# Performance work log

Hardware: AMD Instinct MI355X
Metric: run time of the kernel (lower is better)

The kernel has to match this reference:

```python
import jax, jax.numpy as jnp
import numpy as np

HIDDEN = 128
M_DIM = 128
N_NODES = 50000
N_EDGES = 600000

def _linear_params(key, fan_in, fan_out):
    k1, k2 = jax.random.split(key)
    bound = 1.0 / np.sqrt(fan_in)
    W = jax.random.uniform(k1, (fan_in, fan_out), jnp.float32, -bound, bound)
    b = jax.random.uniform(k2, (fan_out,), jnp.float32, -bound, bound)
    return W, b

def setup_inputs() -> dict:
    key = jax.random.key(0)
    ks = jax.random.split(key, 10)
    h = jax.random.normal(ks[0], (N_NODES, HIDDEN), jnp.float32)
    x = jax.random.normal(ks[1], (N_NODES, 3), jnp.float32)
    edge_index = jax.random.randint(ks[2], (2, N_EDGES), 0, N_NODES, jnp.int64)
    We1, be1 = _linear_params(ks[3], 2 * HIDDEN + 1, M_DIM)
    We2, be2 = _linear_params(ks[4], M_DIM, M_DIM)
    Wg, bg = _linear_params(ks[5], M_DIM, 1)
    Wn1, bn1 = _linear_params(ks[6], HIDDEN + M_DIM, HIDDEN)
    Wn2, bn2 = _linear_params(ks[7], HIDDEN, HIDDEN)
    Wc1, bc1 = _linear_params(ks[8], M_DIM, M_DIM)
    Wc2, bc2 = _linear_params(ks[9], M_DIM, 1)
    return {"h": h, "x": x, "edge_index": edge_index,
            "We1": We1, "be1": be1, "We2": We2, "be2": be2,
            "Wg": Wg, "bg": bg,
            "Wn1": Wn1, "bn1": bn1, "Wn2": Wn2, "bn2": bn2,
            "Wc1": Wc1, "bc1": bc1, "Wc2": Wc2, "bc2": bc2}

def reference(h, x, edge_index, We1, be1, We2, be2, Wg, bg,
              Wn1, bn1, Wn2, bn2, Wc1, bc1, Wc2, bc2):
    silu = jax.nn.silu
    row, col = edge_index[0], edge_index[1]
    N = h.shape[0]
    # gather endpoints
    x_j = x[row]          # [E, 3]
    x_i = x[col]          # [E, 3]
    coord_diff = x_i - x_j
    dist = jnp.linalg.norm(coord_diff, axis=-1, keepdims=True)  # [E, 1]
    h_j = h[row]          # [E, H]
    h_i = h[col]          # [E, H]
    msg_inputs = jnp.concatenate([h_i, h_j, dist], axis=-1)     # [E, 2H+1]
    # edge MLP: Linear -> SiLU -> Linear -> SiLU
    m_ij = silu(silu(msg_inputs @ We1 + be1) @ We2 + be2)       # [E, M]
    gate = jax.nn.sigmoid(m_ij @ Wg + bg)                       # [E, 1]
    m_ij = m_ij * gate
    # scatter-add aggregation over destination nodes
    m_aggr = jax.ops.segment_sum(m_ij, col, num_segments=N)     # [N, M]
    node_input = jnp.concatenate([h, m_aggr], axis=-1)          # [N, H+M]
    delta_h = silu(node_input @ Wn1 + bn1) @ Wn2 + bn2
    h_out = h + delta_h
    # coordinate update
    coor_weights = (silu(m_ij @ Wc1 + bc1) @ Wc2 + bc2)         # [E, 1]
    coord_updates = coord_diff * coor_weights                   # [E, 3]
    coord_aggr = jax.ops.segment_sum(coord_updates, col, num_segments=N)
    x_out = x + coord_aggr
    return (h_out, x_out)
```

## Files before the change

kernel.cpp:

```cpp
#include <hip/hip_runtime.h>
#include <cmath>

#define HID 128

typedef __attribute__((ext_vector_type(8))) short bf16x8;
typedef __attribute__((ext_vector_type(4))) float f32x4;

__device__ __forceinline__ unsigned short f2bf(float f) {
    union { float f; unsigned int i; } c; c.f = f;
    unsigned int r = c.i + 0x7fffu + ((c.i >> 16) & 1u);
    return (unsigned short)(r >> 16);
}
__device__ __forceinline__ unsigned cvt_pk(float lo, float hi) {
    unsigned r;
    asm("v_cvt_pk_bf16_f32 %0, %1, %2" : "=v"(r) : "v"(lo), "v"(hi));
    return r;
}
__device__ __forceinline__ float silu_f(float v) {
    float t = __builtin_amdgcn_exp2f(-1.44269504f * v);
    return v * __builtin_amdgcn_rcpf(1.0f + t);
}
__device__ __forceinline__ float sigmoid_f(float v) {
    return __builtin_amdgcn_rcpf(1.0f + __builtin_amdgcn_exp2f(-1.44269504f * v));
}
typedef __fp16 fp16x2 __attribute__((ext_vector_type(2)));
__device__ __forceinline__ void atomic_pk_add_f16(void* p, float lo, float hi) {
    union { fp16x2 h; unsigned u; } cv;
    cv.h = __builtin_amdgcn_cvt_pkrtz(lo, hi);
    unsigned long long a = (unsigned long long)p;
    asm volatile("global_atomic_pk_add_f16 %0, %1, off" :: "v"(a), "v"(cv.u) : "memory");
}

__global__ __launch_bounds__(256) void egnn_prep(
    const float* __restrict__ We1, const float* __restrict__ We2,
    const float* __restrict__ Wc1, const float* __restrict__ Wn1,
    const float* __restrict__ Wn2,
    short* __restrict__ We1p, short* __restrict__ We2p, short* __restrict__ Wc1p,
    short* __restrict__ Wn1p, short* __restrict__ Wn2p)
{
    int t = blockIdx.x * 256 + threadIdx.x;
    int frag = t >> 6, lane = t & 63;
    if (frag >= 224) return;
    const float* W; short* dst; int KC, f;
    if (frag < 64)       { W = We1; dst = We1p; KC = 8; f = frag; }
    else if (frag < 96)  { W = We2; dst = We2p; KC = 4; f = frag - 64; }
    else if (frag < 128) { W = Wc1; dst = Wc1p; KC = 4; f = frag - 96; }
    else if (frag < 192) { W = Wn1; dst = Wn1p; KC = 8; f = frag - 128; }
    else                 { W = Wn2; dst = Wn2p; KC = 4; f = frag - 192; }
    int nt = f / KC, kc = f % KC;
    int n = nt * 16 + (lane & 15);
    short* d = dst + (((size_t)nt * KC + kc) * 64 + lane) * 8;
    #pragma unroll
    for (int j = 0; j < 8; ++j) {
        int k = kc * 32 + ((lane >> 4) << 2) + (j & 3) + ((j >> 2) << 4);
        d[j] = (short)f2bf(W[(size_t)k * HID + n]);
    }
}

__global__ __launch_bounds__(256) void egnn_edge_mfma(
    const float* __restrict__ h, const float* __restrict__ x,
    const int* __restrict__ ei, int E,
    const short* __restrict__ We1p, const float* __restrict__ We1,
    const float* __restrict__ be1,
    const short* __restrict__ We2p, const float* __restrict__ be2,
    const float* __restrict__ Wg, const float* __restrict__ bg,
    const short* __restrict__ Wc1p, const float* __restrict__ bc1,
    const float* __restrict__ Wc2, const float* __restrict__ bc2,
    short* __restrict__ m16, float* __restrict__ coord_aggr)
{
    __shared__ short sStage[64 * 256];
    __shared__ float s_be1[128], s_w256[128], s_be2[128];
    __shared__ float s_wg[128], s_bc1[128], s_wc2[128];
    __shared__ int   s_col[64], s_row[64];

    const int tid  = threadIdx.x;
    const int lane = tid & 63;
    const int w    = tid >> 6;
    const int l15  = lane & 15;
    const int g    = lane >> 4;
    const int e0   = blockIdx.x * 64;

    if (tid < 64) {
        s_row[tid] = ei[e0 + tid];
        s_col[tid] = ei[E + e0 + tid];
    }
    if (tid < 128) {
        s_be1[tid]  = be1[tid];
        s_w256[tid] = We1[(size_t)256 * HID + tid];
        s_be2[tid]  = be2[tid];
        s_wg[tid]   = Wg[tid];
        s_bc1[tid]  = bc1[tid];
        s_wc2[tid]  = Wc2[tid];
    }
    __syncthreads();

    #pragma unroll
    for (int it = 0; it < 16; ++it) {
        int e = w + 4 * it;
        int q = lane;
        int node = (q < 32) ? s_col[e] : s_row[e];
        float4 v = *(const float4*)&h[(size_t)node * HID + (size_t)(q & 31) * 4];
        uint2 pk;
        pk.x = cvt_pk(v.x, v.y);
        pk.y = cvt_pk(v.z, v.w);
        *(uint2*)((char*)sStage + e * 512 + ((q * 8) ^ ((e & 7) << 4))) = pk;
    }

    const int eloc = w * 16 + l15;
    const int nr = s_row[eloc], nc = s_col[eloc];
    float dx = x[nc * 3 + 0] - x[nr * 3 + 0];
    float dy = x[nc * 3 + 1] - x[nr * 3 + 1];
    float dz = x[nc * 3 + 2] - x[nr * 3 + 2];
    float dist = sqrtf(dx * dx + dy * dy + dz * dz);
    __syncthreads();

    const char* stageRow = (const char*)sStage + eloc * 512;
    const int sw = (eloc & 7) << 4;
    const bf16x8* A1 = (const bf16x8*)We1p;
    const bf16x8* A2 = (const bf16x8*)We2p;
    const bf16x8* A3 = (const bf16x8*)Wc1p;

    f32x4 acc[8];
    #pragma unroll
    for (int mt = 0; mt < 8; ++mt) {
        int f = mt * 16 + g * 4;
        #pragma unroll
        for (int r = 0; r < 4; ++r)
            acc[mt][r] = s_be1[f + r] + dist * s_w256[f + r];
    }
    #pragma unroll
    for (int kc = 0; kc < 8; ++kc) {
        int kb = kc * 64 + g * 8;
        uint2 lo = *(const uint2*)(stageRow + ((kb     ) ^ sw));
        uint2 hi = *(const uint2*)(stageRow + ((kb + 32) ^ sw));
        bf16x8 b; ((uint2*)&b)[0] = lo; ((uint2*)&b)[1] = hi;
        #pragma unroll
        for (int mt = 0; mt < 8; ++mt)
            acc[mt] = __builtin_amdgcn_mfma_f32_16x16x32_bf16(A1[(mt * 8 + kc) * 64 + lane], b, acc[mt], 0, 0, 0);
    }

    bf16x8 Bn[4];
    #pragma unroll
    for (int kc = 0; kc < 4; ++kc) {
        unsigned* d = (unsigned*)&Bn[kc];
        d[0] = cvt_pk(silu_f(acc[2 * kc][0]),     silu_f(acc[2 * kc][1]));
        d[1] = cvt_pk(silu_f(acc[2 * kc][2]),     silu_f(acc[2 * kc][3]));
        d[2] = cvt_pk(silu_f(acc[2 * kc + 1][0]), silu_f(acc[2 * kc + 1][1]));
        d[3] = cvt_pk(silu_f(acc[2 * kc + 1][2]), silu_f(acc[2 * kc + 1][3]));
    }

    f32x4 acc2[8];
    #pragma unroll
    for (int mt = 0; mt < 8; ++mt) {
        int f = mt * 16 + g * 4;
        #pragma unroll
        for (int r = 0; r < 4; ++r) acc2[mt][r] = s_be2[f + r];
    }
    #pragma unroll
    for (int kc = 0; kc < 4; ++kc)
        #pragma unroll
        for (int mt = 0; mt < 8; ++mt)
            acc2[mt] = __builtin_amdgcn_mfma_f32_16x16x32_bf16(A2[(mt * 4 + kc) * 64 + lane], Bn[kc], acc2[mt], 0, 0, 0);

    float gp = 0.f;
    #pragma unroll
    for (int mt = 0; mt < 8; ++mt) {
        int f = mt * 16 + g * 4;
        #pragma unroll
        for (int r = 0; r < 4; ++r) {
            float sv = silu_f(acc2[mt][r]);
            acc2[mt][r] = sv;
            gp += sv * s_wg[f + r];
        }
    }
    gp += __shfl_xor(gp, 16, 64);
    gp += __shfl_xor(gp, 32, 64);
    float gate = sigmoid_f(gp + bg[0]);

    #pragma unroll
    for (int mt = 0; mt < 8; ++mt) {
        f32x4 v;
        #pragma unroll
        for (int r = 0; r < 4; ++r) { acc2[mt][r] *= gate; v[r] = acc2[mt][r]; }
        *(f32x4*)((char*)sStage + eloc * 512 + ((g * 16 + mt * 64) ^ sw)) = v;
    }

    bf16x8 B3[4];
    #pragma unroll
    for (int kc = 0; kc < 4; ++kc) {
        unsigned* d = (unsigned*)&B3[kc];
        d[0] = cvt_pk(acc2[2 * kc][0],     acc2[2 * kc][1]);
        d[1] = cvt_pk(acc2[2 * kc][2],     acc2[2 * kc][3]);
        d[2] = cvt_pk(acc2[2 * kc + 1][0], acc2[2 * kc + 1][1]);
        d[3] = cvt_pk(acc2[2 * kc + 1][2], acc2[2 * kc + 1][3]);
    }

    #pragma unroll
    for (int i = 0; i < 16; ++i) {
        int e = w * 16 + i;
        int c = s_col[e];
        int swE = (e & 7) << 4;
        float2 v = *(const float2*)((const char*)sStage + e * 512 + ((lane * 8) ^ swE));
        atomic_pk_add_f16(m16 + (size_t)c * HID + lane * 2, v.x, v.y);
    }

    f32x4 acc3[8];
    #pragma unroll
    for (int mt = 0; mt < 8; ++mt) {
        int f = mt * 16 + g * 4;
        #pragma unroll
        for (int r = 0; r < 4; ++r) acc3[mt][r] = s_bc1[f + r];
    }
    #pragma unroll
    for (int kc = 0; kc < 4; ++kc)
        #pragma unroll
        for (int mt = 0; mt < 8; ++mt)
            acc3[mt] = __builtin_amdgcn_mfma_f32_16x16x32_bf16(A3[(mt * 4 + kc) * 64 + lane], B3[kc], acc3[mt], 0, 0, 0);

    float cwp = 0.f;
    #pragma unroll
    for (int mt = 0; mt < 8; ++mt) {
        int f = mt * 16 + g * 4;
        #pragma unroll
        for (int r = 0; r < 4; ++r)
            cwp += silu_f(acc3[mt][r]) * s_wc2[f + r];
    }
    cwp += __shfl_xor(cwp, 16, 64);
    cwp += __shfl_xor(cwp, 32, 64);
    float cw = cwp + bc2[0];
    if (g == 0) {
        atomicAdd(&coord_aggr[nc * 3 + 0], dx * cw);
        atomicAdd(&coord_aggr[nc * 3 + 1], dy * cw);
        atomicAdd(&coord_aggr[nc * 3 + 2], dz * cw);
    }
}

__global__ __launch_bounds__(256) void egnn_node_mfma(
    const float* __restrict__ h, const float* __restrict__ x,
    const short* __restrict__ m16, const float* __restrict__ coord_aggr,
    const short* __restrict__ Wn1p, const float* __restrict__ bn1,
    const short* __restrict__ Wn2p, const float* __restrict__ bn2,
    float* __restrict__ h_out, float* __restrict__ x_out, int N)
{
    __shared__ short sStage[64 * 256];
    __shared__ float s_bn1[128], s_bn2[128];

    const int tid  = threadIdx.x;
    const int lane = tid & 63;
    const int w    = tid >> 6;
    const int l15  = lane & 15;
    const int g    = lane >> 4;
    const int n0   = blockIdx.x * 64;

    if (tid < 128) { s_bn1[tid] = bn1[tid]; s_bn2[tid] = bn2[tid]; }

    if (tid < 192) {
        int gi = n0 * 3 + tid;
        if (gi < 3 * N) x_out[gi] = x[gi] + coord_aggr[gi];
    }

    #pragma unroll
    for (int it = 0; it < 16; ++it) {
        int e = w + 4 * it;
        int q = lane;
        int node = min(n0 + e, N - 1);
        uint2 pk;
        if (q < 32) {
            float4 v = *(const float4*)&h[(size_t)node * HID + (size_t)q * 4];
            pk.x = cvt_pk(v.x, v.y);
            pk.y = cvt_pk(v.z, v.w);
        } else {
            uint2 hv = *(const uint2*)((const char*)m16 + (size_t)node * 256 + (size_t)(q & 31) * 8);
            const __fp16* hp = (const __fp16*)&hv;
            pk.x = cvt_pk((float)hp[0], (float)hp[1]);
            pk.y = cvt_pk((float)hp[2], (float)hp[3]);
        }
        *(uint2*)((char*)sStage + e * 512 + ((q * 8) ^ ((e & 7) << 4))) = pk;
    }
    __syncthreads();

    const int nloc = w * 16 + l15;
    const int node = n0 + nloc;
    const char* stageRow = (const char*)sStage + nloc * 512;
    const int sw = (nloc & 7) << 4;
    const bf16x8* A1 = (const bf16x8*)Wn1p;
    const bf16x8* A2 = (const bf16x8*)Wn2p;

    f32x4 acc[8];
    #pragma unroll
    for (int mt = 0; mt < 8; ++mt) {
        int f = mt * 16 + g * 4;
        #pragma unroll
        for (int r = 0; r < 4; ++r) acc[mt][r] = s_bn1[f + r];
    }
    #pragma unroll
    for (int kc = 0; kc < 8; ++kc) {
        int kb = kc * 64 + g * 8;
        uint2 lo = *(const uint2*)(stageRow + ((kb     ) ^ sw));
        uint2 hi = *(const uint2*)(stageRow + ((kb + 32) ^ sw));
        bf16x8 b; ((uint2*)&b)[0] = lo; ((uint2*)&b)[1] = hi;
        #pragma unroll
        for (int mt = 0; mt < 8; ++mt)
            acc[mt] = __builtin_amdgcn_mfma_f32_16x16x32_bf16(A1[(mt * 8 + kc) * 64 + lane], b, acc[mt], 0, 0, 0);
    }

    bf16x8 Bn[4];
    #pragma unroll
    for (int kc = 0; kc < 4; ++kc) {
        unsigned* d = (unsigned*)&Bn[kc];
        d[0] = cvt_pk(silu_f(acc[2 * kc][0]),     silu_f(acc[2 * kc][1]));
        d[1] = cvt_pk(silu_f(acc[2 * kc][2]),     silu_f(acc[2 * kc][3]));
        d[2] = cvt_pk(silu_f(acc[2 * kc + 1][0]), silu_f(acc[2 * kc + 1][1]));
        d[3] = cvt_pk(silu_f(acc[2 * kc + 1][2]), silu_f(acc[2 * kc + 1][3]));
    }

    f32x4 acc2[8];
    #pragma unroll
    for (int mt = 0; mt < 8; ++mt) {
        int f = mt * 16 + g * 4;
        #pragma unroll
        for (int r = 0; r < 4; ++r) acc2[mt][r] = s_bn2[f + r];
    }
    #pragma unroll
    for (int kc = 0; kc < 4; ++kc)
        #pragma unroll
        for (int mt = 0; mt < 8; ++mt)
            acc2[mt] = __builtin_amdgcn_mfma_f32_16x16x32_bf16(A2[(mt * 4 + kc) * 64 + lane], Bn[kc], acc2[mt], 0, 0, 0);

    if (node < N) {
        #pragma unroll
        for (int mt = 0; mt < 8; ++mt) {
            size_t base = (size_t)node * HID + mt * 16 + g * 4;
            float4 hres = *(const float4*)&h[base];
            float4 o;
            o.x = acc2[mt][0] + hres.x;
            o.y = acc2[mt][1] + hres.y;
            o.z = acc2[mt][2] + hres.z;
            o.w = acc2[mt][3] + hres.w;
            *(float4*)&h_out[base] = o;
        }
    }
}

extern "C" void kernel_launch(void* const* d_in, const int* in_sizes, int n_in,
                              void* d_out, int out_size, void* d_ws, size_t ws_size,
                              hipStream_t stream) {
    const float* h   = (const float*)d_in[0];
    const float* x   = (const float*)d_in[1];
    const int*   ei  = (const int*)d_in[2];
    const float* We1 = (const float*)d_in[3];
    const float* be1 = (const float*)d_in[4];
    const float* We2 = (const float*)d_in[5];
    const float* be2 = (const float*)d_in[6];
    const float* Wg  = (const float*)d_in[7];
    const float* bg  = (const float*)d_in[8];
    const float* Wn1 = (const float*)d_in[9];
    const float* bn1 = (const float*)d_in[10];
    const float* Wn2 = (const float*)d_in[11];
    const float* bn2 = (const float*)d_in[12];
    const float* Wc1 = (const float*)d_in[13];
    const float* bc1 = (const float*)d_in[14];
    const float* Wc2 = (const float*)d_in[15];
    const float* bc2 = (const float*)d_in[16];

    const int N = in_sizes[0] / HID;
    const int E = in_sizes[2] / 2;

    short* m16        = (short*)d_ws;
    float* coord_aggr = (float*)(m16 + (size_t)N * HID);
    short* We1p       = (short*)(coord_aggr + (size_t)N * 3);
    short* We2p       = We1p + 256 * 128;
    short* Wc1p       = We2p + 128 * 128;
    short* Wn1p       = Wc1p + 128 * 128;
    short* Wn2p       = Wn1p + 256 * 128;

    (void)hipMemsetAsync(d_ws, 0, (size_t)N * (HID * 2 + 12), stream);

    float* h_out = (float*)d_out;
    float* x_out = h_out + (size_t)N * HID;

    egnn_prep<<<dim3(56), dim3(256), 0, stream>>>(
        We1, We2, Wc1, Wn1, Wn2, We1p, We2p, Wc1p, Wn1p, Wn2p);
    egnn_edge_mfma<<<dim3((E + 63) / 64), dim3(256), 0, stream>>>(
        h, x, ei, E, We1p, We1, be1, We2p, be2, Wg, bg, Wc1p, bc1, Wc2, bc2,
        m16, coord_aggr);
    egnn_node_mfma<<<dim3((N + 63) / 64), dim3(256), 0, stream>>>(
        h, x, m16, coord_aggr, Wn1p, bn1, Wn2p, bn2, h_out, x_out, N);
}
```

Before: 378.0 us.

## Sort edges by destination and pre-reduce messages before fp16 atomics

Adds a counting sort of edges by destination node (count, single-block scan, scatter), so each edge block sees destination-sorted edges. Consecutive edges with the same destination are summed in registers before the packed fp16 atomic, which cuts atomic traffic. Node features are also pre-packed to bf16 once, which halves gather bytes in the edge and node kernels. The cost is four extra launches, a serial single-block scan over 50k nodes, and a non-deterministic scatter order. Average in-degree is about 12, so runs of repeated destinations inside a 16-edge group are fairly long.

```diff
diff --git a/kernel.cpp b/kernel.cpp
--- a/kernel.cpp
+++ b/kernel.cpp
@@ -24,11 +24,14 @@
     return __builtin_amdgcn_rcpf(1.0f + __builtin_amdgcn_exp2f(-1.44269504f * v));
 }
 typedef __fp16 fp16x2 __attribute__((ext_vector_type(2)));
-__device__ __forceinline__ void atomic_pk_add_f16(void* p, float lo, float hi) {
+__device__ __forceinline__ unsigned pkrtz(float lo, float hi) {
     union { fp16x2 h; unsigned u; } cv;
     cv.h = __builtin_amdgcn_cvt_pkrtz(lo, hi);
+    return cv.u;
+}
+__device__ __forceinline__ void atomic_pk_add_f16_raw(void* p, unsigned u) {
     unsigned long long a = (unsigned long long)p;
-    asm volatile("global_atomic_pk_add_f16 %0, %1, off" :: "v"(a), "v"(cv.u) : "memory");
+    asm volatile("global_atomic_pk_add_f16 %0, %1, off" :: "v"(a), "v"(u) : "memory");
 }
 
 __global__ __launch_bounds__(256) void egnn_prep(
@@ -57,9 +60,67 @@
     }
 }
 
+__global__ __launch_bounds__(256) void egnn_hpack(
+    const float* __restrict__ h, short* __restrict__ h16, int N)
+{
+    int t = blockIdx.x * 256 + threadIdx.x;
+    if (t < N * 32) {
+        float4 v = *(const float4*)(h + (size_t)t * 4);
+        uint2 p; p.x = cvt_pk(v.x, v.y); p.y = cvt_pk(v.z, v.w);
+        *(uint2*)(h16 + (size_t)t * 4) = p;
+    }
+}
+
+__global__ __launch_bounds__(256) void egnn_count(
+    const int* __restrict__ ei, int E, int* __restrict__ cnt)
+{
+    int t = blockIdx.x * 256 + threadIdx.x;
+    if (t < E) atomicAdd(&cnt[ei[E + t]], 1);
+}
+
+__global__ __launch_bounds__(1024) void egnn_scan(
+    const int* __restrict__ cnt, int* __restrict__ cursor, int N)
+{
+    __shared__ int part[1024];
+    int t = threadIdx.x;
+    int chunk = (N + 1023) >> 10;
+    int base = t * chunk;
+    int s = 0;
+    for (int i = 0; i < chunk; ++i) {
+        int idx = base + i;
+        if (idx < N) s += cnt[idx];
+    }
+    part[t] = s;
+    __syncthreads();
+    for (int off = 1; off < 1024; off <<= 1) {
+        int u = (t >= off) ? part[t - off] : 0;
+        __syncthreads();
+        part[t] += u;
+        __syncthreads();
+    }
+    int run = part[t] - s;
+    for (int i = 0; i < chunk; ++i) {
+        int idx = base + i;
+        if (idx < N) { cursor[idx] = run; run += cnt[idx]; }
+    }
+}
+
+__global__ __launch_bounds__(256) void egnn_scatter(
+    const int* __restrict__ ei, int E, int* __restrict__ cursor,
+    int2* __restrict__ sorted)
+{
+    int t = blockIdx.x * 256 + threadIdx.x;
+    if (t < E) {
+        int col = ei[E + t];
+        int pos = atomicAdd(&cursor[col], 1);
+        int2 rc; rc.x = ei[t]; rc.y = col;
+        sorted[pos] = rc;
+    }
+}
+
 __global__ __launch_bounds__(256) void egnn_edge_mfma(
-    const float* __restrict__ h, const float* __restrict__ x,
-    const int* __restrict__ ei, int E,
+    const short* __restrict__ h16, const float* __restrict__ x,
+    const int2* __restrict__ sorted, int E,
     const short* __restrict__ We1p, const float* __restrict__ We1,
     const float* __restrict__ be1,
     const short* __restrict__ We2p, const float* __restrict__ be2,
@@ -79,10 +140,13 @@
     const int l15  = lane & 15;
     const int g    = lane >> 4;
     const int e0   = blockIdx.x * 64;
+    const int ne   = min(64, E - e0);
 
     if (tid < 64) {
-        s_row[tid] = ei[e0 + tid];
-        s_col[tid] = ei[E + e0 + tid];
+        int slot = min(e0 + tid, E - 1);
+        int2 rc = sorted[slot];
+        s_row[tid] = rc.x;
+        s_col[tid] = rc.y;
     }
     if (tid < 128) {
         s_be1[tid]  = be1[tid];
@@ -99,11 +163,8 @@
         int e = w + 4 * it;
         int q = lane;
         int node = (q < 32) ? s_col[e] : s_row[e];
-        float4 v = *(const float4*)&h[(size_t)node * HID + (size_t)(q & 31) * 4];
-        uint2 pk;
-        pk.x = cvt_pk(v.x, v.y);
-        pk.y = cvt_pk(v.z, v.w);
-        *(uint2*)((char*)sStage + e * 512 + ((q * 8) ^ ((e & 7) << 4))) = pk;
+        uint2 v = *(const uint2*)(h16 + (size_t)node * HID + (size_t)(q & 31) * 4);
+        *(uint2*)((char*)sStage + e * 512 + ((q * 8) ^ ((e & 7) << 4))) = v;
     }
 
     const int eloc = w * 16 + l15;
@@ -176,6 +237,7 @@
     gp += __shfl_xor(gp, 16, 64);
     gp += __shfl_xor(gp, 32, 64);
     float gate = sigmoid_f(gp + bg[0]);
+    gate *= (eloc < ne) ? 1.0f : 0.0f;
 
     #pragma unroll
     for (int mt = 0; mt < 8; ++mt) {
@@ -195,13 +257,24 @@
         d[3] = cvt_pk(acc2[2 * kc + 1][2], acc2[2 * kc + 1][3]);
     }
 
-    #pragma unroll
-    for (int i = 0; i < 16; ++i) {
-        int e = w * 16 + i;
-        int c = s_col[e];
-        int swE = (e & 7) << 4;
-        float2 v = *(const float2*)((const char*)sStage + e * 512 + ((lane * 8) ^ swE));
-        atomic_pk_add_f16(m16 + (size_t)c * HID + lane * 2, v.x, v.y);
+    __syncthreads();
+
+    {
+        int fp = tid & 63;
+        int rg = tid >> 6;
+        float ax = 0.f, ay = 0.f;
+        int d = s_col[rg * 16];
+        #pragma unroll
+        for (int i = 0; i < 16; ++i) {
+            int e = rg * 16 + i;
+            float2 v = *(const float2*)((const char*)sStage + e * 512 + ((fp * 8) ^ ((e & 7) << 4)));
+            ax += v.x; ay += v.y;
+            int dn = (i < 15) ? s_col[e + 1] : -1;
+            if (dn != d) {
+                atomic_pk_add_f16_raw(m16 + (size_t)d * HID + fp * 2, pkrtz(ax, ay));
+                ax = 0.f; ay = 0.f; d = dn;
+            }
+        }
     }
 
     f32x4 acc3[8];
@@ -228,7 +301,7 @@
     cwp += __shfl_xor(cwp, 16, 64);
     cwp += __shfl_xor(cwp, 32, 64);
     float cw = cwp + bc2[0];
-    if (g == 0) {
+    if (g == 0 && eloc < ne) {
         atomicAdd(&coord_aggr[nc * 3 + 0], dx * cw);
         atomicAdd(&coord_aggr[nc * 3 + 1], dy * cw);
         atomicAdd(&coord_aggr[nc * 3 + 2], dz * cw);
@@ -236,7 +309,8 @@
 }
 
 __global__ __launch_bounds__(256) void egnn_node_mfma(
-    const float* __restrict__ h, const float* __restrict__ x,
+    const float* __restrict__ h, const short* __restrict__ h16,
+    const float* __restrict__ x,
     const short* __restrict__ m16, const float* __restrict__ coord_aggr,
     const short* __restrict__ Wn1p, const float* __restrict__ bn1,
     const short* __restrict__ Wn2p, const float* __restrict__ bn2,
@@ -266,9 +340,7 @@
         int node = min(n0 + e, N - 1);
         uint2 pk;
         if (q < 32) {
-            float4 v = *(const float4*)&h[(size_t)node * HID + (size_t)q * 4];
-            pk.x = cvt_pk(v.x, v.y);
-            pk.y = cvt_pk(v.z, v.w);
+            pk = *(const uint2*)(h16 + (size_t)node * HID + (size_t)q * 4);
         } else {
             uint2 hv = *(const uint2*)((const char*)m16 + (size_t)node * 256 + (size_t)(q & 31) * 8);
             const __fp16* hp = (const __fp16*)&hv;
@@ -366,24 +438,34 @@
     const int N = in_sizes[0] / HID;
     const int E = in_sizes[2] / 2;
 
-    short* m16        = (short*)d_ws;
-    float* coord_aggr = (float*)(m16 + (size_t)N * HID);
-    short* We1p       = (short*)(coord_aggr + (size_t)N * 3);
-    short* We2p       = We1p + 256 * 128;
-    short* Wc1p       = We2p + 128 * 128;
-    short* Wn1p       = Wc1p + 128 * 128;
-    short* Wn2p       = Wn1p + 256 * 128;
-
-    (void)hipMemsetAsync(d_ws, 0, (size_t)N * (HID * 2 + 12), stream);
+    char* p = (char*)d_ws;
+    short* m16        = (short*)p;  p += (size_t)N * 256;
+    float* coord_aggr = (float*)p;  p += (size_t)N * 12;
+    int*   cnt        = (int*)p;    p += (size_t)N * 4;
+    int*   cursor     = (int*)p;    p += (size_t)N * 4;
+    p = (char*)(((uintptr_t)p + 7) & ~(uintptr_t)7);
+    int2*  sorted     = (int2*)p;   p += (size_t)E * 8;
+    short* h16        = (short*)p;  p += (size_t)N * 256;
+    short* We1p       = (short*)p;  p += 256 * 128 * 2;
+    short* We2p       = (short*)p;  p += 128 * 128 * 2;
+    short* Wc1p       = (short*)p;  p += 128 * 128 * 2;
+    short* Wn1p       = (short*)p;  p += 256 * 128 * 2;
+    short* Wn2p       = (short*)p;  p += 128 * 128 * 2;
+
+    (void)hipMemsetAsync(d_ws, 0, (size_t)N * 272, stream);
 
     float* h_out = (float*)d_out;
     float* x_out = h_out + (size_t)N * HID;
 
     egnn_prep<<<dim3(56), dim3(256), 0, stream>>>(
         We1, We2, Wc1, Wn1, Wn2, We1p, We2p, Wc1p, Wn1p, Wn2p);
+    egnn_hpack<<<dim3((N * 32 + 255) / 256), dim3(256), 0, stream>>>(h, h16, N);
+    egnn_count<<<dim3((E + 255) / 256), dim3(256), 0, stream>>>(ei, E, cnt);
+    egnn_scan<<<dim3(1), dim3(1024), 0, stream>>>(cnt, cursor, N);
+    egnn_scatter<<<dim3((E + 255) / 256), dim3(256), 0, stream>>>(ei, E, cursor, sorted);
     egnn_edge_mfma<<<dim3((E + 63) / 64), dim3(256), 0, stream>>>(
-        h, x, ei, E, We1p, We1, be1, We2p, be2, Wg, bg, Wc1p, bc1, Wc2, bc2,
+        h16, x, sorted, E, We1p, We1, be1, We2p, be2, Wg, bg, Wc1p, bc1, Wc2, bc2,
         m16, coord_aggr);
     egnn_node_mfma<<<dim3((N + 63) / 64), dim3(256), 0, stream>>>(
-        h, x, m16, coord_aggr, Wn1p, bn1, Wn2p, bn2, h_out, x_out, N);
-}
+        h, h16, x, m16, coord_aggr, Wn1p, bn1, Wn2p, bn2, h_out, x_out, N);
+}
```

Measured after the change: 609.5 us. +61.2%, slower.
